# Optimization experiments

Hardware: AMD Instinct MI355X
Metric: run time of the kernel (lower is better)

Reference implementation:

```python
import jax, jax.numpy as jnp
import numpy as np

TOPK_CONF = 100   # cfg.nms_top_k_conf
TOPK_IOU = 15     # cfg.nms_top_k_iou
IOU_GAUSS = (32, 32)  # cfg.iou_gauss_dim
EPS = 1e-6        # cfg.positive


def unnormal_gaussian(mask_shape, loc):
    """loc: [..., 4] = (cx, cy, w, h) in [0,1). Returns [..., H, W] unnormalized gaussians."""
    H, W = mask_shape
    ys = (jnp.arange(H, dtype=loc.dtype) + 0.5) / H  # [H]
    xs = (jnp.arange(W, dtype=loc.dtype) + 0.5) / W  # [W]
    cx, cy = loc[..., 0], loc[..., 1]
    sx = jnp.abs(loc[..., 2]) * 0.5 + 1e-3
    sy = jnp.abs(loc[..., 3]) * 0.5 + 1e-3
    dx2 = (xs - cx[..., None]) ** 2 / (2.0 * sx[..., None] ** 2)  # [..., W]
    dy2 = (ys - cy[..., None]) ** 2 / (2.0 * sy[..., None] ** 2)  # [..., H]
    return jnp.exp(-(dy2[..., :, None] + dx2[..., None, :]))      # [..., H, W]


def setup_inputs() -> dict:
    key = jax.random.key(0)
    k1, k2, k3, k4, k5 = jax.random.split(key, 5)
    B, P, C, M = 4, 19248, 81, 32
    original = jax.random.normal(k1, (B, 3, 550, 550), dtype=jnp.float32)
    loc = jax.random.uniform(k2, (B, P, 4), dtype=jnp.float32)  # cx,cy,w,h in [0,1)
    conf = jax.random.normal(k3, (B, P, C), dtype=jnp.float32)
    mask = jax.random.normal(k4, (B, P, M), dtype=jnp.float32)
    proto = jax.random.normal(k5, (B, 138, 138, M), dtype=jnp.float32)
    return {"original": original, "loc": loc, "conf": conf, "mask": mask, "proto": proto}


def reference(original, loc, conf, mask, proto):
    B, H, W = original.shape[0], original.shape[2], original.shape[3]
    # class-1 foreground confidence after softmax over classes
    conf1 = jax.nn.softmax(conf, axis=2)[:, :, 1]  # [B, P]

    # ---- detect(): top-k by conf, pairwise gaussian IoU, keep lowest-overlap boxes ----
    order = jnp.argsort(-conf1, axis=-1)[:, :TOPK_CONF]                    # [B, K]
    sconf = jnp.take_along_axis(conf1, order, axis=1)                      # [B, K]
    sloc = jnp.take_along_axis(loc, order[..., None], axis=1)              # [B, K, 4]
    smask = jnp.take_along_axis(mask, order[..., None], axis=1)            # [B, K, Mdim]

    gauss = unnormal_gaussian(IOU_GAUSS, sloc)                             # [B, K, G, G]
    g_rows = gauss[:, None, :, :, :]                                       # broadcast [B,1,K,G,G]
    g_cols = gauss[:, :, None, :, :]                                       # broadcast [B,K,1,G,G]
    inter = jnp.sum(jnp.minimum(g_rows, g_cols), axis=(-2, -1))            # [B, K, K]
    union = jnp.sum(jnp.maximum(g_rows, g_cols), axis=(-2, -1))            # [B, K, K]
    gauss_iou = inter / union
    iou_max = jnp.max(jnp.triu(gauss_iou, k=1), axis=1)                    # [B, K]
    keep = jnp.argsort(iou_max, axis=-1)[:, :TOPK_IOU]                     # [B, Kk]

    kloc = jnp.take_along_axis(sloc, keep[..., None], axis=1)              # [B, Kk, 4]
    kmask = jnp.take_along_axis(smask, keep[..., None], axis=1)            # [B, Kk, Mdim]
    kconf = jnp.take_along_axis(sconf, keep, axis=1)                       # [B, Kk]

    # ---- VarianceLoss ----
    Hp, Wp = proto.shape[1], proto.shape[2]
    ug = unnormal_gaussian((Hp, Wp), kloc)                                 # [B, Kk, Hp, Wp]
    assembled = jax.nn.sigmoid(jnp.einsum('bhwm,bkm->bkhw', proto, kmask)) # lincomb + sigmoid
    attention = assembled * ug
    mask_conf = attention * kconf[:, :, None, None]                        # einsum('abcd,ab->abcd')
    denom = jnp.sum(mask_conf, axis=1, keepdims=True) + EPS
    final_conf = 1.0 - jnp.sum(mask_conf ** 2 / denom, axis=1)             # [B, Hp, Wp]
    final_conf = jnp.where(jnp.isnan(final_conf), 0.0, final_conf)

    resized = jax.image.resize(final_conf, (B, H, W), method='bilinear')   # [B, H, W]
    total_conf = jnp.sum(resized, axis=0)                                  # [H, W]
    weighted_mean = jnp.einsum('bchw,bhw->chw', original, resized)         # [C, H, W]
    squared_diff = (original - weighted_mean) ** 2
    weighted_diff = squared_diff * resized[:, None, :, :]                  # einsum('abcd,acd->abcd')
    weighted_var = weighted_diff / (total_conf + EPS)
    return jnp.sum(weighted_var) / 100.0
```

## Files before the change

kernel.cpp:

```cpp
#include <hip/hip_runtime.h>
#include <math.h>

#define B 4
#define P 19248
#define C 81
#define M 32
#define K1 100
#define K2 15
#define G 32
#define HP 138
#define HO 550
#define FEPS 1e-6f
#define NLOC 19

#define NBUCKET 8192
#define CAP 2048

#define TI 16
#define NT 7
#define NTP 28
#define CH 128
#define NCH 8
#define SP 132

__global__ void k_conf1(const float* __restrict__ conf, float* __restrict__ conf1,
                        unsigned int* __restrict__ ioumax, float* __restrict__ out) {
    if (blockIdx.x == 0) {
        for (int t = threadIdx.x; t < B * K1; t += 256) ioumax[t] = 0u;
        if (threadIdx.x == 0) out[0] = 0.f;
    }
    int gid  = blockIdx.x * blockDim.x + threadIdx.x;
    int wave = gid >> 6;
    int lane = threadIdx.x & 63;
    if (wave >= B * P) return;
    const float* row = conf + (size_t)wave * C;
    float x0 = (lane < C)      ? row[lane]      : -INFINITY;
    float x1 = (lane + 64 < C) ? row[lane + 64] : -INFINITY;
    float m = fmaxf(x0, x1);
#pragma unroll
    for (int o = 32; o; o >>= 1) m = fmaxf(m, __shfl_xor(m, o, 64));
    float s = 0.f;
    if (lane < C)      s += expf(x0 - m);
    if (lane + 64 < C) s += expf(x1 - m);
#pragma unroll
    for (int o = 32; o; o >>= 1) s += __shfl_xor(s, o, 64);
    if (lane == 0) conf1[wave] = expf(row[1] - m) / s;
}

__global__ __launch_bounds__(1024) void k_top100(
    const float* __restrict__ conf1, const float* __restrict__ loc,
    const float* __restrict__ mask,
    float* __restrict__ sconf, float* __restrict__ sloc,
    float* __restrict__ smask) {
    int b = blockIdx.x;
    int tid = threadIdx.x;
    const float* c1 = conf1 + (size_t)b * P;

    __shared__ unsigned int hist[NBUCKET];
    __shared__ unsigned int gsum_[1024];
    __shared__ unsigned int g2[64];
    __shared__ unsigned long long keys[CAP];
    __shared__ int s_T;
    __shared__ int s_cnt;
    __shared__ int   s_order[K1];
    __shared__ float s_conf[K1];

    for (int i = tid; i < NBUCKET; i += 1024) hist[i] = 0;
    if (tid == 0) s_cnt = 0;
    __syncthreads();

    unsigned int mybits[NLOC];
#pragma unroll
    for (int s = 0; s < NLOC; ++s) {
        int p = tid + s * 1024;
        mybits[s] = (p < P) ? __float_as_uint(c1[p]) : 0u;
        if (p < P) atomicAdd(&hist[mybits[s] >> 17], 1u);
    }
    __syncthreads();

    {
        unsigned int gs = 0;
#pragma unroll
        for (int i = 0; i < 8; ++i) gs += hist[tid * 8 + i];
        gsum_[tid] = gs;
    }
    __syncthreads();
    if (tid < 64) {
        unsigned int gs = 0;
#pragma unroll
        for (int i = 0; i < 16; ++i) gs += gsum_[tid * 16 + i];
        g2[tid] = gs;
    }
    __syncthreads();

    if (tid == 0) {
        int cum = 0;
        int S = 63;
        for (; S > 0; --S) {
            if (cum + (int)g2[S] >= K1) break;
            cum += (int)g2[S];
        }
        int gI = S * 16 + 15;
        for (; gI > S * 16; --gI) {
            if (cum + (int)gsum_[gI] >= K1) break;
            cum += (int)gsum_[gI];
        }
        int T = gI * 8 + 7;
        for (; T > gI * 8; --T) {
            cum += (int)hist[T];
            if (cum >= K1) break;
        }
        s_T = T;
    }
    __syncthreads();

    int T = s_T;
#pragma unroll
    for (int s = 0; s < NLOC; ++s) {
        int p = tid + s * 1024;
        if (p < P && (int)(mybits[s] >> 17) >= T) {
            int pos = atomicAdd(&s_cnt, 1);
            if (pos < CAP)
                keys[pos] = ((unsigned long long)mybits[s] << 32)
                          | (unsigned int)(0xFFFFFFFFu - (unsigned int)p);
        }
    }
    __syncthreads();
    int nc = min(s_cnt, CAP);

    if (tid < nc) {
        unsigned long long mk = keys[tid];
        int rank = 0;
        for (int i = 0; i < nc; ++i) rank += (keys[i] > mk);
        if (rank < K1) {
            unsigned int bits = (unsigned int)(mk >> 32);
            int idx = (int)(0xFFFFFFFFu - (unsigned int)(mk & 0xFFFFFFFFu));
            s_order[rank] = idx;
            s_conf[rank] = __uint_as_float(bits);
        }
    }
    __syncthreads();

    for (int t = tid; t < K1; t += 1024) {
        sconf[b * K1 + t] = s_conf[t];
    }
    for (int t = tid; t < K1 * 4; t += 1024) {
        int k = t >> 2, d = t & 3;
        sloc[(b * K1 + k) * 4 + d] = loc[((size_t)b * P + s_order[k]) * 4 + d];
    }
    for (int t = tid; t < K1 * M; t += 1024) {
        int k = t >> 5, d = t & 31;
        smask[(b * K1 + k) * M + d] = mask[((size_t)b * P + s_order[k]) * M + d];
    }
}

__global__ void k_gauss(const float* __restrict__ sloc, float* __restrict__ gauss) {
    int bk = blockIdx.x;
    const float* l = sloc + bk * 4;
    float cx = l[0], cy = l[1];
    float sx = fabsf(l[2]) * 0.5f + 0.001f;
    float sy = fabsf(l[3]) * 0.5f + 0.001f;
    float dsx = 2.f * sx * sx;
    float dsy = 2.f * sy * sy;
    for (int p = threadIdx.x; p < G * G; p += 256) {
        int y = p >> 5, x = p & 31;
        float xs = (x + 0.5f) / (float)G;
        float ys = (y + 0.5f) / (float)G;
        float dx2 = (xs - cx) * (xs - cx) / dsx;
        float dy2 = (ys - cy) * (ys - cy) / dsy;
        gauss[(size_t)bk * (G * G) + p] = expf(-(dy2 + dx2));
    }
}

__global__ __launch_bounds__(256) void k_iou_tile(
    const float* __restrict__ gauss, float2* __restrict__ pbuf) {
    int ch = blockIdx.x;
    int tp = blockIdx.y;
    int b  = blockIdx.z;
    int ti = 0, rem = tp;
    while (rem >= NT - ti) { rem -= NT - ti; ++ti; }
    int tj = ti + rem;

    __shared__ __align__(16) float As[TI][SP];
    __shared__ __align__(16) float Bs[TI][SP];

    int tid = threadIdx.x;
    for (int idx = tid; idx < TI * (CH / 4); idx += 256) {
        int g = idx >> 5, v = idx & 31;
        int gi = ti * TI + g;
        float4 f = make_float4(0.f, 0.f, 0.f, 0.f);
        if (gi < K1)
            f = *(const float4*)(gauss + ((size_t)(b * K1 + gi) << 10) + ch * CH + v * 4);
        *(float4*)(&As[g][v * 4]) = f;
        int gj = tj * TI + g;
        float4 h = make_float4(0.f, 0.f, 0.f, 0.f);
        if (gj < K1)
            h = *(const float4*)(gauss + ((size_t)(b * K1 + gj) << 10) + ch * CH + v * 4);
        *(float4*)(&Bs[g][v * 4]) = h;
    }
    __syncthreads();

    int li = tid >> 4, lj = tid & 15;
    const float4* ar = (const float4*)(&As[li][0]);
    const float4* br = (const float4*)(&Bs[lj][0]);
    float inter = 0.f, uni = 0.f;
#pragma unroll
    for (int p = 0; p < CH / 4; ++p) {
        float4 a = ar[p], c = br[p];
        inter += fminf(a.x, c.x) + fminf(a.y, c.y)
               + fminf(a.z, c.z) + fminf(a.w, c.w);
        uni   += fmaxf(a.x, c.x) + fmaxf(a.y, c.y)
               + fmaxf(a.z, c.z) + fmaxf(a.w, c.w);
    }
    pbuf[(((size_t)(b * NTP + tp)) * NCH + ch) * 256 + tid] = make_float2(inter, uni);
}

__global__ __launch_bounds__(256) void k_combine(
    const float2* __restrict__ pbuf, unsigned int* __restrict__ ioumax) {
    int tp = blockIdx.x;
    int b  = blockIdx.y;
    int tid = threadIdx.x;
    int ti = 0, rem = tp;
    while (rem >= NT - ti) { rem -= NT - ti; ++ti; }
    int tj = ti + rem;
    int li = tid >> 4, lj = tid & 15;
    int i = ti * TI + li, j = tj * TI + lj;

    size_t base = ((size_t)(b * NTP + tp)) * NCH * 256 + tid;
    float I = 0.f, U = 0.f;
#pragma unroll
    for (int ch = 0; ch < NCH; ++ch) {
        float2 f = pbuf[base + (size_t)ch * 256];
        I += f.x;
        U += f.y;
    }
    if (i < j && j < K1) {
        float iou = I / U;
        atomicMax(&ioumax[b * K1 + j], __float_as_uint(iou));
    }
}

__global__ __launch_bounds__(256) void k_fconf(
    const float* __restrict__ proto, const unsigned int* __restrict__ ioumax,
    const float* __restrict__ sloc, const float* __restrict__ smask,
    const float* __restrict__ sconf, float* __restrict__ fconf) {
    int b = blockIdx.y;
    int px0 = blockIdx.x * 256;
    int tid = threadIdx.x;
    __shared__ float s_pv[256][M + 1];
    __shared__ float s_km[K2][M];
    __shared__ float s_loc[K2][4];
    __shared__ float s_cf[K2];
    __shared__ int s_keep[K2];

    if (tid < 64) {
        int lane = tid;
        float v0 = (lane < K1)      ? __uint_as_float(ioumax[b * K1 + lane])      : INFINITY;
        float v1 = (lane + 64 < K1) ? __uint_as_float(ioumax[b * K1 + lane + 64]) : INFINITY;
        for (int k = 0; k < K2; ++k) {
            float bv; int bi;
            if (v0 <= v1) { bv = v0; bi = lane; }
            else          { bv = v1; bi = lane + 64; }
#pragma unroll
            for (int o = 32; o; o >>= 1) {
                float ov = __shfl_xor(bv, o, 64);
                int   oi = __shfl_xor(bi, o, 64);
                if (ov < bv || (ov == bv && oi < bi)) { bv = ov; bi = oi; }
            }
            if (bi == lane)           v0 = INFINITY;
            else if (bi == lane + 64) v1 = INFINITY;
            if (lane == 0) s_keep[k] = bi;
        }
    }
    __syncthreads();

    for (int t = tid; t < K2 * M; t += 256) {
        int k = t >> 5, d = t & 31;
        s_km[k][d] = smask[(b * K1 + s_keep[k]) * M + d];
    }
    for (int t = tid; t < K2 * 4; t += 256) {
        int k = t >> 2, d = t & 3;
        s_loc[k][d] = sloc[(b * K1 + s_keep[k]) * 4 + d];
    }
    if (tid < K2) s_cf[tid] = sconf[b * K1 + s_keep[tid]];

    int nvalid = min(256, HP * HP - px0);
    const float4* pr4 = (const float4*)(proto + ((size_t)b * (HP * HP) + px0) * M);
    for (int idx = tid; idx < nvalid * (M / 4); idx += 256) {
        float4 f = pr4[idx];
        int q = idx >> 3, v = idx & 7;
        s_pv[q][v * 4 + 0] = f.x;
        s_pv[q][v * 4 + 1] = f.y;
        s_pv[q][v * 4 + 2] = f.z;
        s_pv[q][v * 4 + 3] = f.w;
    }
    __syncthreads();

    if (tid < nvalid) {
        int p = px0 + tid;
        int h = p / HP, w = p % HP;
        float pv[M];
#pragma unroll
        for (int m = 0; m < M; ++m) pv[m] = s_pv[tid][m];
        float ys = (h + 0.5f) / (float)HP;
        float xs = (w + 0.5f) / (float)HP;
        float sum_a = 0.f, sum_a2 = 0.f;
#pragma unroll 1
        for (int k = 0; k < K2; ++k) {
            float d = 0.f;
#pragma unroll
            for (int m = 0; m < M; ++m) d += pv[m] * s_km[k][m];
            float sig = 1.f / (1.f + expf(-d));
            float cx = s_loc[k][0], cy = s_loc[k][1];
            float sx = fabsf(s_loc[k][2]) * 0.5f + 0.001f;
            float sy = fabsf(s_loc[k][3]) * 0.5f + 0.001f;
            float dx2 = (xs - cx) * (xs - cx) / (2.f * sx * sx);
            float dy2 = (ys - cy) * (ys - cy) / (2.f * sy * sy);
            float ug = expf(-(dy2 + dx2));
            float a = sig * ug * s_cf[k];
            sum_a  += a;
            sum_a2 += a * a;
        }
        float fin = 1.f - sum_a2 / (sum_a + FEPS);
        if (!(fin == fin)) fin = 0.f;
        fconf[(size_t)b * HP * HP + p] = fin;
    }
}

__global__ void k_reduce(const float* __restrict__ fconf, const float* __restrict__ original,
                         float* __restrict__ out) {
    int idx = blockIdx.x * 256 + threadIdx.x;
    float contrib = 0.f;
    if (idx < HO * HO) {
        int y = idx / HO, x = idx % HO;
        const float scale = (float)HP / (float)HO;
        float fy = (y + 0.5f) * scale - 0.5f;
        float fx = (x + 0.5f) * scale - 0.5f;
        float y0f = floorf(fy), x0f = floorf(fx);
        float wy = fy - y0f, wx = fx - x0f;
        int y0 = (int)y0f, x0 = (int)x0f;
        int iy0 = max(y0, 0), iy1 = min(y0 + 1, HP - 1);
        int ix0 = max(x0, 0), ix1 = min(x0 + 1, HP - 1);
        float r[B];
#pragma unroll
        for (int b = 0; b < B; ++b) {
            const float* F = fconf + (size_t)b * HP * HP;
            float v00 = F[iy0 * HP + ix0], v01 = F[iy0 * HP + ix1];
            float v10 = F[iy1 * HP + ix0], v11 = F[iy1 * HP + ix1];
            r[b] = (1.f - wy) * ((1.f - wx) * v00 + wx * v01)
                 +        wy  * ((1.f - wx) * v10 + wx * v11);
        }
        float t = r[0] + r[1] + r[2] + r[3];
        float s = 0.f;
#pragma unroll
        for (int c = 0; c < 3; ++c) {
            float o[B], wm = 0.f;
#pragma unroll
            for (int b = 0; b < B; ++b) {
                o[b] = original[(((size_t)b * 3 + c) * HO + y) * HO + x];
                wm += o[b] * r[b];
            }
#pragma unroll
            for (int b = 0; b < B; ++b) {
                float d = o[b] - wm;
                s += d * d * r[b];
            }
        }
        contrib = s / (t + FEPS);
    }
    __shared__ float red[256];
    red[threadIdx.x] = contrib;
    __syncthreads();
    for (int off = 128; off; off >>= 1) {
        if (threadIdx.x < off) red[threadIdx.x] += red[threadIdx.x + off];
        __syncthreads();
    }
    if (threadIdx.x == 0) atomicAdd(out, red[0] * 0.01f);
}

extern "C" void kernel_launch(void* const* d_in, const int* in_sizes, int n_in,
                              void* d_out, int out_size, void* d_ws, size_t ws_size,
                              hipStream_t stream) {
    (void)in_sizes; (void)n_in; (void)out_size; (void)ws_size;
    const float* original = (const float*)d_in[0];
    const float* loc      = (const float*)d_in[1];
    const float* conf     = (const float*)d_in[2];
    const float* mask     = (const float*)d_in[3];
    const float* proto    = (const float*)d_in[4];
    float* out = (float*)d_out;

    char* ws = (char*)d_ws;
    size_t off = 0;
    auto alloc = [&](size_t bytes) -> void* {
        void* p = ws + off;
        off += (bytes + 255) & ~(size_t)255;
        return p;
    };
    float* conf1        = (float*)alloc((size_t)B * P * sizeof(float));
    float* sconf        = (float*)alloc((size_t)B * K1 * sizeof(float));
    float* sloc         = (float*)alloc((size_t)B * K1 * 4 * sizeof(float));
    float* smask        = (float*)alloc((size_t)B * K1 * M * sizeof(float));
    float* gauss        = (float*)alloc((size_t)B * K1 * G * G * sizeof(float));
    float2* pbuf        = (float2*)alloc((size_t)B * NTP * NCH * 256 * sizeof(float2));
    unsigned int* iomax = (unsigned int*)alloc((size_t)B * K1 * sizeof(unsigned int));
    float* fconf        = (float*)alloc((size_t)B * HP * HP * sizeof(float));

    k_conf1<<<(B * P) / 4, 256, 0, stream>>>(conf, conf1, iomax, out);
    k_top100<<<B, 1024, 0, stream>>>(conf1, loc, mask, sconf, sloc, smask);
    k_gauss<<<B * K1, 256, 0, stream>>>(sloc, gauss);
    dim3 g4(NCH, NTP, B);
    k_iou_tile<<<g4, 256, 0, stream>>>(gauss, pbuf);
    dim3 g4b(NTP, B);
    k_combine<<<g4b, 256, 0, stream>>>(pbuf, iomax);
    dim3 g6((HP * HP + 255) / 256, B);
    k_fconf<<<g6, 256, 0, stream>>>(proto, iomax, sloc, smask, sconf, fconf);
    k_reduce<<<(HO * HO + 255) / 256, 256, 0, stream>>>(fconf, original, out);
}
```

Baseline: 167.3 us.

## Fuse gaussian generation into top-k and IoU combine into tile kernel

The gaussian-map kernel is folded into the end of the top-k kernel, and the separate combine kernel is replaced by a last-block-done pattern: each IoU tile block bumps an atomic counter, and the final block for a tile pair sums the partials and does the atomicMax. The serial threshold search in top-k becomes a wave-level scan using shuffles and ballots. This cuts two kernel launches and a serial single-thread loop. In exchange, only 4 blocks now compute all the gaussians, and extra fences and atomics are added.

```diff
diff --git a/kernel.cpp b/kernel.cpp
--- a/kernel.cpp
+++ b/kernel.cpp
@@ -24,9 +24,11 @@
 #define SP 132
 
 __global__ void k_conf1(const float* __restrict__ conf, float* __restrict__ conf1,
-                        unsigned int* __restrict__ ioumax, float* __restrict__ out) {
+                        unsigned int* __restrict__ ioumax, int* __restrict__ iocnt,
+                        float* __restrict__ out) {
     if (blockIdx.x == 0) {
         for (int t = threadIdx.x; t < B * K1; t += 256) ioumax[t] = 0u;
+        for (int t = threadIdx.x; t < B * NTP; t += 256) iocnt[t] = 0;
         if (threadIdx.x == 0) out[0] = 0.f;
     }
     int gid  = blockIdx.x * blockDim.x + threadIdx.x;
@@ -51,7 +53,7 @@
     const float* __restrict__ conf1, const float* __restrict__ loc,
     const float* __restrict__ mask,
     float* __restrict__ sconf, float* __restrict__ sloc,
-    float* __restrict__ smask) {
+    float* __restrict__ smask, float* __restrict__ gauss) {
     int b = blockIdx.x;
     int tid = threadIdx.x;
     const float* c1 = conf1 + (size_t)b * P;
@@ -64,6 +66,7 @@
     __shared__ int s_cnt;
     __shared__ int   s_order[K1];
     __shared__ float s_conf[K1];
+    __shared__ float s_sloc[K1][4];
 
     for (int i = tid; i < NBUCKET; i += 1024) hist[i] = 0;
     if (tid == 0) s_cnt = 0;
@@ -93,24 +96,35 @@
     }
     __syncthreads();
 
-    if (tid == 0) {
-        int cum = 0;
-        int S = 63;
-        for (; S > 0; --S) {
-            if (cum + (int)g2[S] >= K1) break;
-            cum += (int)g2[S];
-        }
-        int gI = S * 16 + 15;
-        for (; gI > S * 16; --gI) {
-            if (cum + (int)gsum_[gI] >= K1) break;
-            cum += (int)gsum_[gI];
-        }
-        int T = gI * 8 + 7;
-        for (; T > gI * 8; --T) {
-            cum += (int)hist[T];
-            if (cum >= K1) break;
-        }
-        s_T = T;
+    if (tid < 64) {
+        unsigned int o2 = g2[tid], v2 = o2;
+#pragma unroll
+        for (int o = 1; o < 64; o <<= 1) {
+            unsigned int t = __shfl_down(v2, o, 64);
+            if (tid + o < 64) v2 += t;
+        }
+        unsigned long long m2 = __ballot(v2 >= K1);
+        int S = 63 - __clzll(m2);
+        int cum = (int)__shfl(v2, S, 64) - (int)__shfl(o2, S, 64);
+        unsigned int o1 = (tid < 16) ? gsum_[S * 16 + tid] : 0u, v1 = o1;
+#pragma unroll
+        for (int o = 1; o < 16; o <<= 1) {
+            unsigned int t = __shfl_down(v1, o, 64);
+            if (tid + o < 16) v1 += t;
+        }
+        unsigned int m1 = (unsigned int)__ballot(tid < 16 && cum + (int)v1 >= K1) & 0xFFFFu;
+        int gIl = 31 - __clz(m1);
+        int gI = S * 16 + gIl;
+        cum += (int)__shfl(v1, gIl, 64) - (int)__shfl(o1, gIl, 64);
+        unsigned int o0 = (tid < 8) ? hist[gI * 8 + tid] : 0u, v0 = o0;
+#pragma unroll
+        for (int o = 1; o < 8; o <<= 1) {
+            unsigned int t = __shfl_down(v0, o, 64);
+            if (tid + o < 8) v0 += t;
+        }
+        unsigned int m0 = (unsigned int)__ballot(tid < 8 && cum + (int)v0 >= K1) & 0xFFu;
+        int Tl = 31 - __clz(m0);
+        if (tid == 0) s_T = gI * 8 + Tl;
     }
     __syncthreads();
 
@@ -146,34 +160,35 @@
     }
     for (int t = tid; t < K1 * 4; t += 1024) {
         int k = t >> 2, d = t & 3;
-        sloc[(b * K1 + k) * 4 + d] = loc[((size_t)b * P + s_order[k]) * 4 + d];
+        float v = loc[((size_t)b * P + s_order[k]) * 4 + d];
+        s_sloc[k][d] = v;
+        sloc[(b * K1 + k) * 4 + d] = v;
     }
     for (int t = tid; t < K1 * M; t += 1024) {
         int k = t >> 5, d = t & 31;
         smask[(b * K1 + k) * M + d] = mask[((size_t)b * P + s_order[k]) * M + d];
     }
-}
-
-__global__ void k_gauss(const float* __restrict__ sloc, float* __restrict__ gauss) {
-    int bk = blockIdx.x;
-    const float* l = sloc + bk * 4;
-    float cx = l[0], cy = l[1];
-    float sx = fabsf(l[2]) * 0.5f + 0.001f;
-    float sy = fabsf(l[3]) * 0.5f + 0.001f;
-    float dsx = 2.f * sx * sx;
-    float dsy = 2.f * sy * sy;
-    for (int p = threadIdx.x; p < G * G; p += 256) {
-        int y = p >> 5, x = p & 31;
+    __syncthreads();
+
+#pragma unroll 1
+    for (int k = 0; k < K1; ++k) {
+        float cx = s_sloc[k][0], cy = s_sloc[k][1];
+        float sx = fabsf(s_sloc[k][2]) * 0.5f + 0.001f;
+        float sy = fabsf(s_sloc[k][3]) * 0.5f + 0.001f;
+        float dsx = 2.f * sx * sx;
+        float dsy = 2.f * sy * sy;
+        int y = tid >> 5, x = tid & 31;
         float xs = (x + 0.5f) / (float)G;
         float ys = (y + 0.5f) / (float)G;
         float dx2 = (xs - cx) * (xs - cx) / dsx;
         float dy2 = (ys - cy) * (ys - cy) / dsy;
-        gauss[(size_t)bk * (G * G) + p] = expf(-(dy2 + dx2));
+        gauss[((size_t)(b * K1 + k) << 10) + tid] = expf(-(dy2 + dx2));
     }
 }
 
 __global__ __launch_bounds__(256) void k_iou_tile(
-    const float* __restrict__ gauss, float2* __restrict__ pbuf) {
+    const float* __restrict__ gauss, float2* __restrict__ pbuf,
+    int* __restrict__ iocnt, unsigned int* __restrict__ ioumax) {
     int ch = blockIdx.x;
     int tp = blockIdx.y;
     int b  = blockIdx.z;
@@ -183,6 +198,7 @@
 
     __shared__ __align__(16) float As[TI][SP];
     __shared__ __align__(16) float Bs[TI][SP];
+    __shared__ int s_last;
 
     int tid = threadIdx.x;
     for (int idx = tid; idx < TI * (CH / 4); idx += 256) {
@@ -212,31 +228,32 @@
         uni   += fmaxf(a.x, c.x) + fmaxf(a.y, c.y)
                + fmaxf(a.z, c.z) + fmaxf(a.w, c.w);
     }
-    pbuf[(((size_t)(b * NTP + tp)) * NCH + ch) * 256 + tid] = make_float2(inter, uni);
-}
-
-__global__ __launch_bounds__(256) void k_combine(
-    const float2* __restrict__ pbuf, unsigned int* __restrict__ ioumax) {
-    int tp = blockIdx.x;
-    int b  = blockIdx.y;
-    int tid = threadIdx.x;
-    int ti = 0, rem = tp;
-    while (rem >= NT - ti) { rem -= NT - ti; ++ti; }
-    int tj = ti + rem;
-    int li = tid >> 4, lj = tid & 15;
-    int i = ti * TI + li, j = tj * TI + lj;
-
-    size_t base = ((size_t)(b * NTP + tp)) * NCH * 256 + tid;
-    float I = 0.f, U = 0.f;
-#pragma unroll
-    for (int ch = 0; ch < NCH; ++ch) {
-        float2 f = pbuf[base + (size_t)ch * 256];
-        I += f.x;
-        U += f.y;
-    }
-    if (i < j && j < K1) {
-        float iou = I / U;
-        atomicMax(&ioumax[b * K1 + j], __float_as_uint(iou));
+    size_t slot = ((size_t)(b * NTP + tp)) * NCH + ch;
+    pbuf[slot * 256 + tid] = make_float2(inter, uni);
+
+    __syncthreads();
+    if (tid == 0) {
+        __threadfence();
+        int prev = atomicAdd(&iocnt[b * NTP + tp], 1);
+        s_last = (prev == NCH - 1);
+    }
+    __syncthreads();
+
+    if (s_last) {
+        __threadfence();
+        size_t base = ((size_t)(b * NTP + tp)) * NCH * 256 + tid;
+        float I = 0.f, U = 0.f;
+#pragma unroll
+        for (int c = 0; c < NCH; ++c) {
+            float2 f = pbuf[base + (size_t)c * 256];
+            I += f.x;
+            U += f.y;
+        }
+        int i = ti * TI + li, j = tj * TI + lj;
+        if (i < j && j < K1) {
+            float iou = I / U;
+            atomicMax(&ioumax[b * K1 + j], __float_as_uint(iou));
+        }
     }
 }
 
@@ -403,15 +420,13 @@
     float* gauss        = (float*)alloc((size_t)B * K1 * G * G * sizeof(float));
     float2* pbuf        = (float2*)alloc((size_t)B * NTP * NCH * 256 * sizeof(float2));
     unsigned int* iomax = (unsigned int*)alloc((size_t)B * K1 * sizeof(unsigned int));
+    int* iocnt          = (int*)alloc((size_t)B * NTP * sizeof(int));
     float* fconf        = (float*)alloc((size_t)B * HP * HP * sizeof(float));
 
-    k_conf1<<<(B * P) / 4, 256, 0, stream>>>(conf, conf1, iomax, out);
-    k_top100<<<B, 1024, 0, stream>>>(conf1, loc, mask, sconf, sloc, smask);
-    k_gauss<<<B * K1, 256, 0, stream>>>(sloc, gauss);
+    k_conf1<<<(B * P) / 4, 256, 0, stream>>>(conf, conf1, iomax, iocnt, out);
+    k_top100<<<B, 1024, 0, stream>>>(conf1, loc, mask, sconf, sloc, smask, gauss);
     dim3 g4(NCH, NTP, B);
-    k_iou_tile<<<g4, 256, 0, stream>>>(gauss, pbuf);
-    dim3 g4b(NTP, B);
-    k_combine<<<g4b, 256, 0, stream>>>(pbuf, iomax);
+    k_iou_tile<<<g4, 256, 0, stream>>>(gauss, pbuf, iocnt, iomax);
     dim3 g6((HP * HP + 255) / 256, B);
     k_fconf<<<g6, 256, 0, stream>>>(proto, iomax, sloc, smask, sconf, fconf);
     k_reduce<<<(HO * HO + 255) / 256, 256, 0, stream>>>(fconf, original, out);
```

After: 250.4 us. 49.6% more time.
